# Optimization experiments

Hardware: AMD Instinct MI355X
Metric: run time of the kernel (lower is better)

## Reference

```python
import jax, jax.numpy as jnp
import numpy as np

D, H, G, HD = 2048, 16, 4, 128  # d_model, num_heads, num_groups, head_dim
B, S = 2, 2048


def _rope(x):
    # x: [B, heads, S, HD]; RoPE with concat(freqs, freqs) layout (rotate_half style)
    seq = x.shape[2]
    inv_freq = 1.0 / (10000.0 ** (jnp.arange(0, HD, 2, dtype=jnp.float32) / HD))  # [HD/2]
    t = jnp.arange(seq, dtype=jnp.float32)
    freqs = t[:, None] * inv_freq[None, :]              # [S, HD/2]
    emb = jnp.concatenate([freqs, freqs], axis=-1)      # [S, HD]
    cos = jnp.cos(emb)[None, None]                      # [1,1,S,HD]
    sin = jnp.sin(emb)[None, None]
    x1, x2 = jnp.split(x, 2, axis=-1)
    rot = jnp.concatenate([-x2, x1], axis=-1)           # rotate_half
    return x * cos + rot * sin


def setup_inputs() -> dict:
    key = jax.random.key(0)
    ks = jax.random.split(key, 5)
    x = jax.random.normal(ks[0], (B, S, D), dtype=jnp.float32)
    # weights stored as [in, out] so y = x @ W (equivalent to torch Linear with W^T)
    Wq = jax.random.normal(ks[1], (D, D), dtype=jnp.float32) * 0.02
    Wk = jax.random.normal(ks[2], (D, G * HD), dtype=jnp.float32) * 0.02
    Wv = jax.random.normal(ks[3], (D, G * HD), dtype=jnp.float32) * 0.02
    Wo = jax.random.normal(ks[4], (D, D), dtype=jnp.float32) * 0.02
    # causal mask: True = masked (matches torch masked_fill semantics)
    mask = ~jnp.tril(jnp.ones((S, S), dtype=bool))[None, None]  # [1,1,S,S]
    return {"x": x, "Wq": Wq, "Wk": Wk, "Wv": Wv, "Wo": Wo, "mask": mask}


def reference(x, Wq, Wk, Wv, Wo, mask):
    b, s, _ = x.shape
    q = (x @ Wq).reshape(b, s, H, HD).transpose(0, 2, 1, 3)   # [B,H,S,HD]
    k = (x @ Wk).reshape(b, s, G, HD).transpose(0, 2, 1, 3)   # [B,G,S,HD]
    v = (x @ Wv).reshape(b, s, G, HD).transpose(0, 2, 1, 3)   # [B,G,S,HD]
    q = _rope(q)
    k = _rope(k)
    # GQA: repeat_interleave KV groups across heads
    k = jnp.repeat(k, H // G, axis=1)                         # [B,H,S,HD]
    v = jnp.repeat(v, H // G, axis=1)
    scale = jnp.float32(1.0 / np.sqrt(HD))
    scores = jnp.einsum('bhqd,bhkd->bhqk', q, k) * scale      # [B,H,S,S]
    scores = jnp.where(mask, jnp.float32(-1e9), scores)
    attn = jax.nn.softmax(scores, axis=-1)
    ctx = jnp.einsum('bhqk,bhkd->bhqd', attn, v)              # [B,H,S,HD]
    ctx = ctx.transpose(0, 2, 1, 3).reshape(b, s, D)
    return ctx @ Wo
```

## Files before the change

### kernel.cpp

```cpp
#include <hip/hip_runtime.h>
#include <hip/hip_bf16.h>
#include <math.h>

#define BB 2
#define SS 2048
#define DD 2048
#define HH 16
#define GG 4
#define HDIM 128
#define DKV (GG * HDIM)
#define MS (BB * SS)
#define QKVS 3072

typedef __attribute__((ext_vector_type(8))) short bf16x8;
typedef __attribute__((ext_vector_type(4))) float f32x4;
typedef __attribute__((ext_vector_type(4))) unsigned int u32x4;

#if __has_builtin(__builtin_amdgcn_exp2f)
#define EXP2F __builtin_amdgcn_exp2f
#else
#define EXP2F exp2f
#endif

__device__ __forceinline__ ushort f2bf(float x) {
    __hip_bfloat16 b = __float2bfloat16(x);
    return *(ushort*)&b;
}
__device__ __forceinline__ float bf2f(ushort u) {
    __hip_bfloat16 b;
    *(ushort*)&b = u;
    return __bfloat162float(b);
}

#define GLOAD_LDS(src, dst)                                                        \
    __builtin_amdgcn_global_load_lds(                                              \
        (const __attribute__((address_space(1))) unsigned int*)(src),              \
        (__attribute__((address_space(3))) unsigned int*)(dst), 16, 0, 0)

#define WAITV(n) asm volatile("s_waitcnt vmcnt(" #n ")" ::: "memory")

__global__ __launch_bounds__(256) void prep4(const float* __restrict__ x,
                                             const float* __restrict__ Wq,
                                             const float* __restrict__ Wk,
                                             const float* __restrict__ Wv,
                                             const float* __restrict__ Wo,
                                             ushort* __restrict__ xh,
                                             ushort* __restrict__ WqkvT,
                                             ushort* __restrict__ WoT) {
    __shared__ ushort tile[32][33];
    const int z = blockIdx.z;
    if (z == 4) {
        int idx = (blockIdx.y * 64 + blockIdx.x) * 256 + threadIdx.x;
        const float4* p = (const float4*)x + (size_t)idx * 2;
        float4 a = p[0], b = p[1];
        float v[8] = {a.x, a.y, a.z, a.w, b.x, b.y, b.z, b.w};
        ushort r[8];
#pragma unroll
        for (int j = 0; j < 8; ++j) r[j] = f2bf(v[j]);
        *((u32x4*)xh + idx) = *(u32x4*)r;
        return;
    }
    if ((z == 1 || z == 2) && blockIdx.x >= DKV / 32) return;
    const float* W = (z == 0) ? Wq : (z == 1) ? Wk : (z == 2) ? Wv : Wo;
    ushort* WT = (z == 3) ? WoT
                          : WqkvT + ((z == 0) ? (size_t)0
                                              : (z == 1) ? (size_t)DD * DD
                                                         : (size_t)(DD + DKV) * DD);
    const int N = (z == 1 || z == 2) ? DKV : DD;
    const int tx = threadIdx.x & 31, ty = threadIdx.x >> 5;
    const int n0 = blockIdx.x * 32, k0 = blockIdx.y * 32;
#pragma unroll
    for (int i = 0; i < 4; ++i)
        tile[ty + i * 8][tx] = f2bf(W[(size_t)(k0 + ty + i * 8) * N + n0 + tx]);
    __syncthreads();
#pragma unroll
    for (int i = 0; i < 4; ++i)
        WT[(size_t)(n0 + ty + i * 8) * DD + k0 + tx] = tile[tx][ty + i * 8];
}

__global__ __launch_bounds__(256) void rope_tv(ushort* __restrict__ QKV,
                                               ushort* __restrict__ VT) {
    __shared__ ushort tile[32][33];
    const int id = blockIdx.x;
    if (id < 2560) {
        int idx = id * 256 + threadIdx.x;
        int oct = idx & 7;
        int hh = (idx >> 3) % 20;
        int row = idx / (8 * 20);
        int s = row & (SS - 1);
        int colOff = (hh < 16) ? hh * HDIM : 2048 + (hh - 16) * HDIM;
        size_t base = (size_t)row * QKVS + colOff + oct * 8;
        u32x4 lo = *(u32x4*)&QKV[base];
        u32x4 hi = *(u32x4*)&QKV[base + 64];
        ushort* lp = (ushort*)&lo;
        ushort* hp = (ushort*)&hi;
        ushort ro[8], rh[8];
#pragma unroll
        for (int j = 0; j < 8; ++j) {
            int i = oct * 8 + j;
            float inv = exp2f((float)i * -0.2076205059304601f);
            float ang = (float)s * inv;
            float c, sn;
            __sincosf(ang, &sn, &c);
            float x1 = bf2f(lp[j]), x2 = bf2f(hp[j]);
            ro[j] = f2bf(x1 * c - x2 * sn);
            rh[j] = f2bf(x2 * c + x1 * sn);
        }
        *(u32x4*)&QKV[base] = *(u32x4*)ro;
        *(u32x4*)&QKV[base + 64] = *(u32x4*)rh;
        return;
    }
    const int lid = id - 2560;
    const int tx = threadIdx.x & 31, ty = threadIdx.x >> 5;
    const int d0 = (lid & 15) * 32;
    const int k0 = ((lid >> 4) & 63) * 32;
    const int b = lid >> 10;
#pragma unroll
    for (int i = 0; i < 4; ++i)
        tile[ty + i * 8][tx] =
            QKV[(size_t)(b * SS + k0 + ty + i * 8) * QKVS + 2560 + d0 + tx];
    __syncthreads();
    const int posl = ((tx & 12) << 1) | ((tx & 16) >> 2) | (tx & 3);
#pragma unroll
    for (int i = 0; i < 4; ++i)
        VT[((size_t)b * DKV + d0 + ty + i * 8) * SS + k0 + posl] = tile[tx][ty + i * 8];
}

template <int BN, bool OUT_BF16>
__global__ __launch_bounds__(512) void gemm8(const ushort* __restrict__ A,
                                             const ushort* __restrict__ BT,
                                             void* __restrict__ Cout,
                                             int M, int N, int K) {
    constexpr int ABUF = 128 * 32;
    constexpr int BBUF = BN * 32;
    constexpr int NWC = BN / 64;
    constexpr int NWM = 8 / NWC;
    constexpr int ROWS = 128 / NWM;
    constexpr int MFR = ROWS / 16;
    __shared__ ushort As[3 * ABUF];
    __shared__ ushort Bs[3 * BBUF];

    const int t = threadIdx.x;
    const int w = t >> 6, l = t & 63;
    const int lm = l & 15, lw = l >> 4;
    const int wr = w / NWC, wc = w % NWC;
    const int nx = gridDim.x;
    const int bid = blockIdx.y * nx + blockIdx.x;
    const int cpx = (nx * gridDim.y) >> 3;
    const int swb = (bid & 7) * cpx + (bid >> 3);
    const int bm = (swb / nx) * 128, bn = (swb % nx) * BN;

    const int NT = K >> 5;
    const int swzc = (lw ^ ((lm >> 1) & 3)) * 8;

    const int ar0 = t >> 2, ac0 = (t & 3) ^ ((ar0 >> 1) & 3);
    const ushort* a0 = A + (size_t)(bm + ar0) * K + ac0 * 8;
    const int br0 = t >> 2, bc0 = (t & 3) ^ ((br0 >> 1) & 3);
    const ushort* b0 = BT + (size_t)(bn + br0) * K + bc0 * 8;
    const int br1 = (t + 512) >> 2, bc1 = ((t + 512) & 3) ^ ((br1 >> 1) & 3);
    const ushort* b1 = BT + (size_t)(bn + br1) * K + bc1 * 8;

    auto STAGE = [&](int slot) {
        GLOAD_LDS(a0, &As[slot * ABUF + t * 8]);
        a0 += 32;
        GLOAD_LDS(b0, &Bs[slot * BBUF + t * 8]);
        b0 += 32;
        if constexpr (BN == 256) {
            GLOAD_LDS(b1, &Bs[slot * BBUF + (t + 512) * 8]);
            b1 += 32;
        }
    };

    f32x4 acc[MFR][4];
#pragma unroll
    for (int m = 0; m < MFR; ++m)
#pragma unroll
        for (int n = 0; n < 4; ++n) acc[m][n] = (f32x4){0.f, 0.f, 0.f, 0.f};

    STAGE(0);
    STAGE(1);
    int cs = 0, ps = 2;

#pragma unroll 1
    for (int kt = 0; kt < NT; ++kt) {
        if (kt + 1 < NT) {
            if constexpr (BN == 256) WAITV(3); else WAITV(2);
        } else {
            WAITV(0);
        }
        __builtin_amdgcn_s_barrier();
        if (kt + 2 < NT) STAGE(ps);

        const ushort* Ab = &As[cs * ABUF];
        const ushort* Bb = &Bs[cs * BBUF];
        bf16x8 bfr[4], af[MFR];
#pragma unroll
        for (int n = 0; n < 4; ++n)
            bfr[n] = *(const bf16x8*)&Bb[(wc * 64 + n * 16 + lm) * 32 + swzc];
#pragma unroll
        for (int i = 0; i < MFR; ++i)
            af[i] = *(const bf16x8*)&Ab[(wr * ROWS + i * 16 + lm) * 32 + swzc];
        __builtin_amdgcn_s_setprio(1);
#pragma unroll
        for (int i = 0; i < MFR; ++i)
#pragma unroll
            for (int n = 0; n < 4; ++n)
                acc[i][n] = __builtin_amdgcn_mfma_f32_16x16x32_bf16(af[i], bfr[n], acc[i][n], 0, 0, 0);
        __builtin_amdgcn_s_setprio(0);

        cs = (cs == 2) ? 0 : cs + 1;
        ps = (ps == 2) ? 0 : ps + 1;
    }

#pragma unroll
    for (int m = 0; m < MFR; ++m)
#pragma unroll
        for (int n = 0; n < 4; ++n)
#pragma unroll
            for (int r = 0; r < 4; ++r) {
                int row = bm + wr * ROWS + m * 16 + lw * 4 + r;
                int col = bn + wc * 64 + n * 16 + lm;
                if (OUT_BF16)
                    ((ushort*)Cout)[(size_t)row * N + col] = f2bf(acc[m][n][r]);
                else
                    ((float*)Cout)[(size_t)row * N + col] = acc[m][n][r];
            }
}

#define SCL 0.08838834764831845f
#define CEXP 0.1275296340545927f
#define THRRAW 90.50966799187809f

__global__ __launch_bounds__(512) void attn_mfma(const ushort* __restrict__ QKV,
                                                 const ushort* __restrict__ VT,
                                                 ushort* __restrict__ Ctx) {
    __shared__ ushort Ks[2][128 * 128];
    __shared__ ushort Vs[2][128 * 128];
    const int t = threadIdx.x;
    const int w = t >> 6;
    const int l = t & 63;
    const int lm = l & 15, lw = l >> 4;
    const int bid = blockIdx.x;
    const int g = bid & 3;
    const int b = (bid >> 2) & 1;
    const int within = bid >> 3;
    const int xq = within & 7;
    const int h = g * 4 + (within >> 3);
    const int swz = (lm & 7) << 3;

    const ushort* kbase = QKV + (size_t)(b * SS) * QKVS + 2048 + g * HDIM;
    const ushort* vbase = VT + ((size_t)b * DKV + g * HDIM) * SS;

    const short one_bf = (short)0x3F80;
    const bf16x8 ones = {one_bf, one_bf, one_bf, one_bf, one_bf, one_bf, one_bf, one_bf};

    int krr[4], koo[4];
#pragma unroll
    for (int it = 0; it < 4; ++it) {
        int c = t + it * 512;
        krr[it] = c >> 4;
        koo[it] = (c & 15) ^ (krr[it] & 7);
    }

#pragma unroll 1
    for (int phase = 0; phase < 2; ++phase) {
        const int qt = (phase == 0) ? xq : (15 - xq);
        const int q0 = qt * 128;
        const int qw = q0 + w * 16;
        const int q = qw + lm;
        const int ntiles = qt + 1;

        const ushort* ks[4];
        const ushort* vs[4];
#pragma unroll
        for (int it = 0; it < 4; ++it) {
            ks[it] = kbase + (size_t)krr[it] * QKVS + koo[it] * 8;
            vs[it] = vbase + (size_t)krr[it] * SS + koo[it] * 8;
        }

        bf16x8 qa[4];
        {
            const ushort* qp = QKV + (size_t)(b * SS + qw + lm) * QKVS + h * HDIM + lw * 8;
#pragma unroll
            for (int kk = 0; kk < 4; ++kk)
                qa[kk] = *(const bf16x8*)(qp + kk * 32);
        }

        f32x4 acc[8];
#pragma unroll
        for (int d = 0; d < 8; ++d) acc[d] = (f32x4){0.f, 0.f, 0.f, 0.f};
        f32x4 accl = (f32x4){0.f, 0.f, 0.f, 0.f};
        float m = -INFINITY;

#pragma unroll
        for (int it = 0; it < 4; ++it) {
            GLOAD_LDS(ks[it], &Ks[0][(t + it * 512) * 8]);
            ks[it] += 128 * QKVS;
            GLOAD_LDS(vs[it], &Vs[0][(t + it * 512) * 8]);
            vs[it] += 128;
        }
        asm volatile("s_waitcnt vmcnt(0)" ::: "memory");
        __builtin_amdgcn_s_barrier();

#pragma unroll 1
        for (int tile = 0; tile < ntiles; ++tile) {
            const int cur = tile & 1;
            const int kv0 = tile * 128;
            const bool more = (tile + 1 < ntiles);
            if (more) {
                ushort* kd = &Ks[cur ^ 1][0];
                ushort* vd = &Vs[cur ^ 1][0];
#pragma unroll
                for (int it = 0; it < 4; ++it) {
                    GLOAD_LDS(ks[it], kd + (t + it * 512) * 8);
                    ks[it] += 128 * QKVS;
                    GLOAD_LDS(vs[it], vd + (t + it * 512) * 8);
                    vs[it] += 128;
                }
            }

            f32x4 sfT[8];
#pragma unroll
            for (int kvb = 0; kvb < 8; ++kvb) sfT[kvb] = (f32x4){0.f, 0.f, 0.f, 0.f};
            __builtin_amdgcn_s_setprio(1);
#pragma unroll
            for (int kvb = 0; kvb < 8; ++kvb)
#pragma unroll
                for (int kk = 0; kk < 4; ++kk) {
                    bf16x8 kb = *(const bf16x8*)&Ks[cur][(kvb * 16 + lm) * 128 + ((kk * 32 + lw * 8) ^ swz)];
                    sfT[kvb] = __builtin_amdgcn_mfma_f32_16x16x32_bf16(kb, qa[kk], sfT[kvb], 0, 0, 0);
                }
            __builtin_amdgcn_s_setprio(0);

            if (tile == ntiles - 1) {
#pragma unroll
                for (int kvb = 0; kvb < 8; ++kvb)
#pragma unroll
                    for (int r = 0; r < 4; ++r) {
                        int kv = kv0 + kvb * 16 + lw * 4 + r;
                        if (kv > q) sfT[kvb][r] = -INFINITY;
                    }
            }

            float rm = fmaxf(fmaxf(sfT[0][0], sfT[0][1]), fmaxf(sfT[0][2], sfT[0][3]));
#pragma unroll
            for (int kvb = 1; kvb < 8; ++kvb)
                rm = fmaxf(rm, fmaxf(fmaxf(sfT[kvb][0], sfT[kvb][1]),
                                     fmaxf(sfT[kvb][2], sfT[kvb][3])));
            rm = fmaxf(rm, __shfl_xor(rm, 16));
            rm = fmaxf(rm, __shfl_xor(rm, 32));

            bool stable = (rm - m <= THRRAW);
            if (!__all((int)stable)) {
                float mn = fmaxf(m, rm);
                float alpha_l = EXP2F((m - mn) * CEXP);
                m = mn;
                float ar[4];
#pragma unroll
                for (int r = 0; r < 4; ++r)
                    ar[r] = __shfl(alpha_l, (l & 48) | (lw * 4 + r));
#pragma unroll
                for (int d = 0; d < 8; ++d) {
                    acc[d][0] *= ar[0];
                    acc[d][1] *= ar[1];
                    acc[d][2] *= ar[2];
                    acc[d][3] *= ar[3];
                }
                accl[0] *= ar[0];
                accl[1] *= ar[1];
                accl[2] *= ar[2];
                accl[3] *= ar[3];
            }

            bf16x8 pa[4];
            float mC = m * CEXP;
#pragma unroll
            for (int kvb = 0; kvb < 8; ++kvb)
#pragma unroll
                for (int r = 0; r < 4; ++r) {
                    float pv = EXP2F(fmaf(sfT[kvb][r], CEXP, -mC));
                    pa[kvb >> 1][(kvb & 1) * 4 + r] = (short)f2bf(pv);
                }

            __builtin_amdgcn_s_setprio(1);
#pragma unroll
            for (int kks = 0; kks < 4; ++kks) {
                accl = __builtin_amdgcn_mfma_f32_16x16x32_bf16(pa[kks], ones, accl, 0, 0, 0);
#pragma unroll
                for (int dcol = 0; dcol < 8; ++dcol) {
                    bf16x8 vb = *(const bf16x8*)&Vs[cur][(dcol * 16 + lm) * 128 + ((kks * 32 + lw * 8) ^ swz)];
                    acc[dcol] = __builtin_amdgcn_mfma_f32_16x16x32_bf16(pa[kks], vb, acc[dcol], 0, 0, 0);
                }
            }
            __builtin_amdgcn_s_setprio(0);

            if (more) {
                asm volatile("s_waitcnt vmcnt(0)" ::: "memory");
                __builtin_amdgcn_s_barrier();
            }
        }

        float rinv[4];
#pragma unroll
        for (int r = 0; r < 4; ++r) rinv[r] = 1.f / accl[r];
        ushort* cp = Ctx + (size_t)(b * SS + qw) * DD + h * HDIM;
#pragma unroll
        for (int d = 0; d < 8; ++d)
#pragma unroll
            for (int r = 0; r < 4; ++r)
                cp[(size_t)(lw * 4 + r) * DD + d * 16 + lm] = f2bf(acc[d][r] * rinv[r]);
        __builtin_amdgcn_s_barrier();
    }
}

extern "C" void kernel_launch(void* const* d_in, const int* in_sizes, int n_in,
                              void* d_out, int out_size, void* d_ws, size_t ws_size,
                              hipStream_t stream) {
    const float* x  = (const float*)d_in[0];
    const float* Wq = (const float*)d_in[1];
    const float* Wk = (const float*)d_in[2];
    const float* Wv = (const float*)d_in[3];
    const float* Wo = (const float*)d_in[4];
    float* out = (float*)d_out;

    ushort* xh    = (ushort*)d_ws;
    ushort* QKV   = xh + (size_t)MS * DD;
    ushort* VTb   = QKV + (size_t)MS * QKVS;
    ushort* WqkvT = VTb + (size_t)MS * DKV;
    ushort* WoT   = WqkvT + (size_t)QKVS * DD;
    ushort* Ch    = xh;

    dim3 blk(256);

    prep4<<<dim3(DD / 32, DD / 32, 5), blk, 0, stream>>>(x, Wq, Wk, Wv, Wo, xh, WqkvT, WoT);

    gemm8<128, true><<<dim3(QKVS / 128, MS / 128), dim3(512), 0, stream>>>(xh, WqkvT, QKV, MS, QKVS, DD);

    rope_tv<<<dim3(2560 + 2048), blk, 0, stream>>>(QKV, VTb);

    attn_mfma<<<dim3(256), dim3(512), 0, stream>>>(QKV, VTb, Ch);

    gemm8<128, false><<<dim3(DD / 128, MS / 128), dim3(512), 0, stream>>>(Ch, WoT, out, MS, DD, DD);
}
```

Baseline: 191.5 us.

## Replace triple-buffered K32 GEMM with double-buffered K64 tile pipeline

Rewrites the bf16 MFMA GEMM used for the QKV and output projections. The K step per iteration goes from 32 to 64, with an 8-way XOR swizzle on the wider LDS rows and two buffers instead of three. This halves the number of loop iterations and barriers and gives each wave more MFMAs per sync. In exchange there is less prefetch depth: each stage is waited on right after the compute, so load latency is hidden only by one tile's worth of work.

New measurement: 189.4 us. About the same (-1.1%).

```diff
diff --git a/kernel.cpp b/kernel.cpp
--- a/kernel.cpp
+++ b/kernel.cpp
@@ -126,99 +126,94 @@
         VT[((size_t)b * DKV + d0 + ty + i * 8) * SS + k0 + posl] = tile[tx][ty + i * 8];
 }
 
-template <int BN, bool OUT_BF16>
-__global__ __launch_bounds__(512) void gemm8(const ushort* __restrict__ A,
-                                             const ushort* __restrict__ BT,
-                                             void* __restrict__ Cout,
-                                             int M, int N, int K) {
-    constexpr int ABUF = 128 * 32;
-    constexpr int BBUF = BN * 32;
-    constexpr int NWC = BN / 64;
-    constexpr int NWM = 8 / NWC;
-    constexpr int ROWS = 128 / NWM;
-    constexpr int MFR = ROWS / 16;
-    __shared__ ushort As[3 * ABUF];
-    __shared__ ushort Bs[3 * BBUF];
-
+template <bool OUT_BF16>
+__global__ __launch_bounds__(512) void gemm64(const ushort* __restrict__ A,
+                                              const ushort* __restrict__ BT,
+                                              void* __restrict__ Cout,
+                                              int M, int N, int K) {
+    __shared__ ushort As[2][128 * 64];
+    __shared__ ushort Bs[2][128 * 64];
     const int t = threadIdx.x;
     const int w = t >> 6, l = t & 63;
     const int lm = l & 15, lw = l >> 4;
-    const int wr = w / NWC, wc = w % NWC;
+    const int wr = w >> 1, wc = w & 1;
     const int nx = gridDim.x;
     const int bid = blockIdx.y * nx + blockIdx.x;
     const int cpx = (nx * gridDim.y) >> 3;
     const int swb = (bid & 7) * cpx + (bid >> 3);
-    const int bm = (swb / nx) * 128, bn = (swb % nx) * BN;
-
-    const int NT = K >> 5;
-    const int swzc = (lw ^ ((lm >> 1) & 3)) * 8;
-
-    const int ar0 = t >> 2, ac0 = (t & 3) ^ ((ar0 >> 1) & 3);
-    const ushort* a0 = A + (size_t)(bm + ar0) * K + ac0 * 8;
-    const int br0 = t >> 2, bc0 = (t & 3) ^ ((br0 >> 1) & 3);
-    const ushort* b0 = BT + (size_t)(bn + br0) * K + bc0 * 8;
-    const int br1 = (t + 512) >> 2, bc1 = ((t + 512) & 3) ^ ((br1 >> 1) & 3);
-    const ushort* b1 = BT + (size_t)(bn + br1) * K + bc1 * 8;
-
-    auto STAGE = [&](int slot) {
-        GLOAD_LDS(a0, &As[slot * ABUF + t * 8]);
-        a0 += 32;
-        GLOAD_LDS(b0, &Bs[slot * BBUF + t * 8]);
-        b0 += 32;
-        if constexpr (BN == 256) {
-            GLOAD_LDS(b1, &Bs[slot * BBUF + (t + 512) * 8]);
-            b1 += 32;
-        }
+    const int bm = (swb / nx) * 128, bn = (swb % nx) * 128;
+    const int NT = K >> 6;
+
+    const int rowc = t >> 3, cc = t & 7;
+    const int xb = (cc ^ (rowc & 7)) * 8;
+    const ushort* a0 = A + (size_t)(bm + rowc) * K + xb;
+    const ushort* a1 = A + (size_t)(bm + rowc + 64) * K + xb;
+    const ushort* b0 = BT + (size_t)(bn + rowc) * K + xb;
+    const ushort* b1 = BT + (size_t)(bn + rowc + 64) * K + xb;
+    const int d0 = t * 8, d1 = (t + 512) * 8;
+
+    auto STAGE = [&](int s) {
+        GLOAD_LDS(a0, &As[s][d0]);
+        a0 += 64;
+        GLOAD_LDS(a1, &As[s][d1]);
+        a1 += 64;
+        GLOAD_LDS(b0, &Bs[s][d0]);
+        b0 += 64;
+        GLOAD_LDS(b1, &Bs[s][d1]);
+        b1 += 64;
     };
 
-    f32x4 acc[MFR][4];
-#pragma unroll
-    for (int m = 0; m < MFR; ++m)
+    f32x4 acc[2][4];
+#pragma unroll
+    for (int m = 0; m < 2; ++m)
 #pragma unroll
         for (int n = 0; n < 4; ++n) acc[m][n] = (f32x4){0.f, 0.f, 0.f, 0.f};
 
     STAGE(0);
-    STAGE(1);
-    int cs = 0, ps = 2;
-
+    WAITV(0);
+    __builtin_amdgcn_s_barrier();
+
+    int buf = 0;
 #pragma unroll 1
     for (int kt = 0; kt < NT; ++kt) {
-        if (kt + 1 < NT) {
-            if constexpr (BN == 256) WAITV(3); else WAITV(2);
-        } else {
+        const bool more = (kt + 1 < NT);
+        if (more) STAGE(buf ^ 1);
+
+        bf16x8 af[2][2], bfr[4][2];
+#pragma unroll
+        for (int ks = 0; ks < 2; ++ks) {
+            const int col = (((ks << 2) | lw) ^ (lm & 7)) * 8;
+#pragma unroll
+            for (int n = 0; n < 4; ++n)
+                bfr[n][ks] = *(const bf16x8*)&Bs[buf][(wc * 64 + n * 16 + lm) * 64 + col];
+#pragma unroll
+            for (int i = 0; i < 2; ++i)
+                af[i][ks] = *(const bf16x8*)&As[buf][(wr * 32 + i * 16 + lm) * 64 + col];
+        }
+        __builtin_amdgcn_s_setprio(1);
+#pragma unroll
+        for (int ks = 0; ks < 2; ++ks)
+#pragma unroll
+            for (int i = 0; i < 2; ++i)
+#pragma unroll
+                for (int n = 0; n < 4; ++n)
+                    acc[i][n] = __builtin_amdgcn_mfma_f32_16x16x32_bf16(af[i][ks], bfr[n][ks], acc[i][n], 0, 0, 0);
+        __builtin_amdgcn_s_setprio(0);
+
+        if (more) {
             WAITV(0);
-        }
-        __builtin_amdgcn_s_barrier();
-        if (kt + 2 < NT) STAGE(ps);
-
-        const ushort* Ab = &As[cs * ABUF];
-        const ushort* Bb = &Bs[cs * BBUF];
-        bf16x8 bfr[4], af[MFR];
+            __builtin_amdgcn_s_barrier();
+        }
+        buf ^= 1;
+    }
+
+#pragma unroll
+    for (int m = 0; m < 2; ++m)
 #pragma unroll
         for (int n = 0; n < 4; ++n)
-            bfr[n] = *(const bf16x8*)&Bb[(wc * 64 + n * 16 + lm) * 32 + swzc];
-#pragma unroll
-        for (int i = 0; i < MFR; ++i)
-            af[i] = *(const bf16x8*)&Ab[(wr * ROWS + i * 16 + lm) * 32 + swzc];
-        __builtin_amdgcn_s_setprio(1);
-#pragma unroll
-        for (int i = 0; i < MFR; ++i)
-#pragma unroll
-            for (int n = 0; n < 4; ++n)
-                acc[i][n] = __builtin_amdgcn_mfma_f32_16x16x32_bf16(af[i], bfr[n], acc[i][n], 0, 0, 0);
-        __builtin_amdgcn_s_setprio(0);
-
-        cs = (cs == 2) ? 0 : cs + 1;
-        ps = (ps == 2) ? 0 : ps + 1;
-    }
-
-#pragma unroll
-    for (int m = 0; m < MFR; ++m)
-#pragma unroll
-        for (int n = 0; n < 4; ++n)
 #pragma unroll
             for (int r = 0; r < 4; ++r) {
-                int row = bm + wr * ROWS + m * 16 + lw * 4 + r;
+                int row = bm + wr * 32 + m * 16 + lw * 4 + r;
                 int col = bn + wc * 64 + n * 16 + lm;
                 if (OUT_BF16)
                     ((ushort*)Cout)[(size_t)row * N + col] = f2bf(acc[m][n][r]);
@@ -434,11 +429,11 @@
 
     prep4<<<dim3(DD / 32, DD / 32, 5), blk, 0, stream>>>(x, Wq, Wk, Wv, Wo, xh, WqkvT, WoT);
 
-    gemm8<128, true><<<dim3(QKVS / 128, MS / 128), dim3(512), 0, stream>>>(xh, WqkvT, QKV, MS, QKVS, DD);
+    gemm64<true><<<dim3(QKVS / 128, MS / 128), dim3(512), 0, stream>>>(xh, WqkvT, QKV, MS, QKVS, DD);
 
     rope_tv<<<dim3(2560 + 2048), blk, 0, stream>>>(QKV, VTb);
 
     attn_mfma<<<dim3(256), dim3(512), 0, stream>>>(QKV, VTb, Ch);
 
-    gemm8<128, false><<<dim3(DD / 128, MS / 128), dim3(512), 0, stream>>>(Ch, WoT, out, MS, DD, DD);
-}
+    gemm64<false><<<dim3(DD / 128, MS / 128), dim3(512), 0, stream>>>(Ch, WoT, out, MS, DD, DD);
+}
```
